# Optimization experiments

Hardware: AMD Instinct MI355X
Metric: run time of the kernel (lower is better)

## Reference

```python
import jax, jax.numpy as jnp
import numpy as np

SEG = 20  # patch size


def setup_inputs() -> dict:
    key = jax.random.key(0)
    k1, k2, k3, k4 = jax.random.split(key, 4)
    x = jax.random.uniform(k1, (2, 20, 1, 240, 240), dtype=jnp.float32)  # pixels in [0,1)
    emb_weight = jax.random.normal(k2, (256, 256), dtype=jnp.float32)
    pos_weight = jax.random.normal(k3, (144, 256), dtype=jnp.float32)
    temp_weight = jax.random.normal(k4, (20, 256), dtype=jnp.float32)
    return {"x": x, "emb_weight": emb_weight, "pos_weight": pos_weight, "temp_weight": temp_weight}


def reference(x, emb_weight, pos_weight, temp_weight):
    B, F, C, H, W = x.shape
    hp, wp = H // SEG, W // SEG  # 12, 12 -> 144 patches
    # segment_image: patches ordered row-major over (y, x), each patch flattened as [C, 20, 20]
    patches = x.reshape(B, F, C, hp, SEG, wp, SEG)
    patches = patches.transpose(0, 1, 3, 5, 2, 4, 6).reshape(B, F, hp * wp, C * SEG * SEG)
    idx = (patches * 255.0).astype(jnp.int32)          # truncation, matches .int()
    emb = emb_weight[idx].mean(axis=3)                 # [B, F, 144, 256] mean over pixels in patch
    emb = emb + pos_weight[None, None]                 # positional add
    cls = jnp.zeros((B, F, 1, emb.shape[-1]), emb.dtype)
    out = jnp.concatenate([cls, emb], axis=2)          # [B, F, 145, 256]
    out = out + temp_weight[:F][None, :, None, :]      # temporal add (incl. cls slot)
    return out
```

## Files before the change

kernel.cpp:

```cpp
#include <hip/hip_runtime.h>


#define F_   20
#define HW   240
#define SEG  20
#define PPB  8
#define BPF  18
#define NBLK (40 * BPF)

__device__ __forceinline__ float bf16_to_f32(ushort u) {
    union { uint i; float f; } c; c.i = ((uint)u) << 16; return c.f;
}
__device__ __forceinline__ ushort f32_to_bf16(float v) {
    union { float f; uint i; } c; c.f = v;
    uint u = c.i;
    u += 0x7FFFu + ((u >> 16) & 1u);
    return (ushort)(u >> 16);
}

template<bool BF16> __device__ __forceinline__ float load_in(const void* p, int i) {
    if constexpr (BF16) return bf16_to_f32(((const ushort*)p)[i]);
    else                return ((const float*)p)[i];
}
template<bool BF16> __device__ __forceinline__ void store_out(void* p, int i, float v) {
    if constexpr (BF16) ((ushort*)p)[i] = f32_to_bf16(v);
    else                ((float*)p)[i] = v;
}

__global__ void detect_dtype(const ushort* __restrict__ x, int* __restrict__ flag) {
    if (threadIdx.x == 0) {
        int bad = 0;
        for (int i = 0; i < 256; i += 2) bad += (int)(x[i] > 0x3F80u);
        *flag = (bad == 0) ? 1 : 0;
    }
}

template<bool BF16>
__device__ __forceinline__ void embed_body(
    const void* __restrict__ xg, const void* __restrict__ embg,
    const void* __restrict__ posg, const void* __restrict__ tempg,
    void* __restrict__ outg,
    uint (&cnt)[PPB][256], float (&cntf)[PPB][256])
{
    const int tid  = threadIdx.x;
    const int bf   = blockIdx.x / BPF;
    const int pblk = blockIdx.x % BPF;
    const int p0   = pblk * PPB;
    const int f    = bf % F_;

    #pragma unroll
    for (int i = 0; i < PPB; ++i) cnt[i][tid] = 0u;
    __syncthreads();

    const int xbase = bf * (HW * HW);
    for (int it = 0; it < 13; ++it) {
        int i = tid + it * 256;
        if (i < PPB * 400) {
            int p  = i / 400;
            int q  = i - p * 400;
            int gp = p0 + p;
            int pr = gp / 12, pc = gp - pr * 12;
            int qr = q / SEG, qc = q - qr * SEG;
            float xv = load_in<BF16>(xg, xbase + (pr * SEG + qr) * HW + pc * SEG + qc);
            int idx = (int)(xv * 255.0f);
            idx = idx < 0 ? 0 : (idx > 255 ? 255 : idx);
            atomicAdd(&cnt[p][idx], 1u);
        }
    }
    __syncthreads();

    #pragma unroll
    for (int i = 0; i < PPB; ++i) cntf[i][tid] = (float)cnt[i][tid];
    __syncthreads();

    float acc[PPB] = {};
    #pragma unroll 4
    for (int k = 0; k < 256; ++k) {
        float e = load_in<BF16>(embg, k * 256 + tid);
        #pragma unroll
        for (int m = 0; m < PPB; ++m) acc[m] += cntf[m][k] * e;
    }

    const int obase = bf * (145 * 256);
    const float tadd = load_in<BF16>(tempg, f * 256 + tid);
    if (pblk == 0)
        store_out<BF16>(outg, obase + tid, tadd);
    #pragma unroll
    for (int m = 0; m < PPB; ++m) {
        int gp = p0 + m;
        float val = acc[m] * (1.0f / 400.0f)
                  + load_in<BF16>(posg, gp * 256 + tid) + tadd;
        store_out<BF16>(outg, obase + (1 + gp) * 256 + tid, val);
    }
}

__global__ __launch_bounds__(256) void video_embed_kernel(
    const void* __restrict__ xg, const void* __restrict__ embg,
    const void* __restrict__ posg, const void* __restrict__ tempg,
    void* __restrict__ outg, const int* __restrict__ flag)
{
    __shared__ uint  cnt[PPB][256];
    __shared__ float cntf[PPB][256];
    const bool isbf = (flag == nullptr) ? true : (*flag != 0);
    if (isbf) embed_body<true >(xg, embg, posg, tempg, outg, cnt, cntf);
    else      embed_body<false>(xg, embg, posg, tempg, outg, cnt, cntf);
}

extern "C" void kernel_launch(void* const* d_in, const int* in_sizes, int n_in,
                              void* d_out, int out_size, void* d_ws, size_t ws_size,
                              hipStream_t stream) {
    int* flag = (ws_size >= sizeof(int)) ? (int*)d_ws : nullptr;
    if (flag)
        detect_dtype<<<dim3(1), dim3(64), 0, stream>>>((const ushort*)d_in[0], flag);
    video_embed_kernel<<<dim3(NBLK), dim3(256), 0, stream>>>(
        d_in[0], d_in[1], d_in[2], d_in[3], d_out, flag);
}
```

Measured before the change: 91.95 us.

## Process full patch-row strips per block with vectorized loads and register-tiled histogram GEMM

Each block now handles one full row of 12 patches (a contiguous 20x240 strip), so pixel loads are contiguous float4 reads and the histogram is accumulated directly as float atomics in LDS. The count-times-embedding product is register-tiled: each thread computes 4 output columns for 12 patches over a 64-wide k slice, and the four waves' partial sums are reduced through shared memory. The separate dtype-detection kernel launch is folded into the main kernel. In exchange, LDS use grows substantially (the per-wave partial buffer), which may reduce occupancy, and float atomics replace integer ones.

After: 91.75 us. Within noise of the previous version (-0.2%).

```diff
diff --git a/kernel.cpp b/kernel.cpp
--- a/kernel.cpp
+++ b/kernel.cpp
@@ -4,13 +4,17 @@
 #define F_   20
 #define HW   240
 #define SEG  20
-#define PPB  8
-#define BPF  18
+#define PPB  12
+#define BPF  12
 #define NBLK (40 * BPF)
+#define STRIP (HW * SEG)
 
-__device__ __forceinline__ float bf16_to_f32(ushort u) {
-    union { uint i; float f; } c; c.i = ((uint)u) << 16; return c.f;
+typedef __attribute__((ext_vector_type(4))) float float4_t;
+
+__device__ __forceinline__ float bits_f32(uint u) {
+    union { uint i; float f; } c; c.i = u; return c.f;
 }
+__device__ __forceinline__ float bf16_to_f32(ushort u) { return bits_f32(((uint)u) << 16); }
 __device__ __forceinline__ ushort f32_to_bf16(float v) {
     union { float f; uint i; } c; c.f = v;
     uint u = c.i;
@@ -18,100 +22,138 @@
     return (ushort)(u >> 16);
 }
 
-template<bool BF16> __device__ __forceinline__ float load_in(const void* p, int i) {
-    if constexpr (BF16) return bf16_to_f32(((const ushort*)p)[i]);
-    else                return ((const float*)p)[i];
+template<bool F32> __device__ __forceinline__ float4_t load4(const void* p, int i) {
+    if constexpr (F32) {
+        return *(const float4_t*)((const float*)p + i);
+    } else {
+        ushort4 u = *(const ushort4*)((const ushort*)p + i);
+        float4_t r;
+        r.x = bf16_to_f32(u.x); r.y = bf16_to_f32(u.y);
+        r.z = bf16_to_f32(u.z); r.w = bf16_to_f32(u.w);
+        return r;
+    }
 }
-template<bool BF16> __device__ __forceinline__ void store_out(void* p, int i, float v) {
-    if constexpr (BF16) ((ushort*)p)[i] = f32_to_bf16(v);
-    else                ((float*)p)[i] = v;
+template<bool F32> __device__ __forceinline__ float load1(const void* p, int i) {
+    if constexpr (F32) return ((const float*)p)[i];
+    else               return bf16_to_f32(((const ushort*)p)[i]);
+}
+template<bool F32> __device__ __forceinline__ void store1(void* p, int i, float v) {
+    if constexpr (F32) ((float*)p)[i] = v;
+    else               ((ushort*)p)[i] = f32_to_bf16(v);
 }
 
-__global__ void detect_dtype(const ushort* __restrict__ x, int* __restrict__ flag) {
-    if (threadIdx.x == 0) {
-        int bad = 0;
-        for (int i = 0; i < 256; i += 2) bad += (int)(x[i] > 0x3F80u);
-        *flag = (bad == 0) ? 1 : 0;
-    }
-}
-
-template<bool BF16>
+template<bool F32>
 __device__ __forceinline__ void embed_body(
     const void* __restrict__ xg, const void* __restrict__ embg,
     const void* __restrict__ posg, const void* __restrict__ tempg,
     void* __restrict__ outg,
-    uint (&cnt)[PPB][256], float (&cntf)[PPB][256])
+    float (&cntf)[PPB][256], float (&part)[PPB][4][256])
 {
     const int tid  = threadIdx.x;
+    const int lane = tid & 63;
+    const int wave = tid >> 6;
     const int bf   = blockIdx.x / BPF;
-    const int pblk = blockIdx.x % BPF;
-    const int p0   = pblk * PPB;
+    const int pr   = blockIdx.x % BPF;
+    const int p0   = pr * 12;
     const int f    = bf % F_;
 
-    #pragma unroll
-    for (int i = 0; i < PPB; ++i) cnt[i][tid] = 0u;
-    __syncthreads();
-
-    const int xbase = bf * (HW * HW);
-    for (int it = 0; it < 13; ++it) {
+    const int xbase = bf * (HW * HW) + pr * STRIP;
+    for (int it = 0; it < 5; ++it) {
         int i = tid + it * 256;
-        if (i < PPB * 400) {
-            int p  = i / 400;
-            int q  = i - p * 400;
-            int gp = p0 + p;
-            int pr = gp / 12, pc = gp - pr * 12;
-            int qr = q / SEG, qc = q - qr * SEG;
-            float xv = load_in<BF16>(xg, xbase + (pr * SEG + qr) * HW + pc * SEG + qc);
-            int idx = (int)(xv * 255.0f);
-            idx = idx < 0 ? 0 : (idx > 255 ? 255 : idx);
-            atomicAdd(&cnt[p][idx], 1u);
+        if (i < STRIP / 4) {
+            int elem = i * 4;
+            int col  = elem % HW;
+            int p    = col / SEG;
+            float4_t v = load4<F32>(xg, xbase + elem);
+            #pragma unroll
+            for (int j = 0; j < 4; ++j) {
+                int idx = (int)(v[j] * 255.0f);
+                idx = idx < 0 ? 0 : (idx > 255 ? 255 : idx);
+                atomicAdd(&cntf[p][idx], 1.0f);
+            }
         }
     }
     __syncthreads();
 
+    const int n0 = lane * 4;
+    const int kbase = wave * 64;
+    float acc[PPB][4];
     #pragma unroll
-    for (int i = 0; i < PPB; ++i) cntf[i][tid] = (float)cnt[i][tid];
+    for (int m = 0; m < PPB; ++m)
+        #pragma unroll
+        for (int c = 0; c < 4; ++c) acc[m][c] = 0.0f;
+
+    #pragma unroll 2
+    for (int kq = 0; kq < 16; ++kq) {
+        const int k = kbase + kq * 4;
+        float e[4][4];
+        #pragma unroll
+        for (int kk = 0; kk < 4; ++kk) {
+            if constexpr (F32) {
+                *(float4_t*)(&e[kk][0]) =
+                    *(const float4_t*)((const float*)embg + (k + kk) * 256 + n0);
+            } else {
+                uint2 u = *(const uint2*)((const ushort*)embg + (k + kk) * 256 + n0);
+                e[kk][0] = bits_f32(u.x << 16);
+                e[kk][1] = bits_f32(u.x & 0xFFFF0000u);
+                e[kk][2] = bits_f32(u.y << 16);
+                e[kk][3] = bits_f32(u.y & 0xFFFF0000u);
+            }
+        }
+        #pragma unroll
+        for (int m = 0; m < PPB; ++m) {
+            float4_t c4 = *(const float4_t*)(&cntf[m][k]);
+            #pragma unroll
+            for (int kk = 0; kk < 4; ++kk)
+                #pragma unroll
+                for (int c = 0; c < 4; ++c)
+                    acc[m][c] += c4[kk] * e[kk][c];
+        }
+    }
+
+    #pragma unroll
+    for (int m = 0; m < PPB; ++m)
+        *(float4_t*)(&part[m][wave][n0]) = *(float4_t*)(&acc[m][0]);
     __syncthreads();
 
-    float acc[PPB] = {};
-    #pragma unroll 4
-    for (int k = 0; k < 256; ++k) {
-        float e = load_in<BF16>(embg, k * 256 + tid);
-        #pragma unroll
-        for (int m = 0; m < PPB; ++m) acc[m] += cntf[m][k] * e;
-    }
-
     const int obase = bf * (145 * 256);
-    const float tadd = load_in<BF16>(tempg, f * 256 + tid);
-    if (pblk == 0)
-        store_out<BF16>(outg, obase + tid, tadd);
+    const float tadd = load1<F32>(tempg, f * 256 + tid);
+    if (pr == 0)
+        store1<F32>(outg, obase + tid, tadd);
     #pragma unroll
     for (int m = 0; m < PPB; ++m) {
+        float s = part[m][0][tid] + part[m][1][tid] + part[m][2][tid] + part[m][3][tid];
         int gp = p0 + m;
-        float val = acc[m] * (1.0f / 400.0f)
-                  + load_in<BF16>(posg, gp * 256 + tid) + tadd;
-        store_out<BF16>(outg, obase + (1 + gp) * 256 + tid, val);
+        float val = s * (1.0f / 400.0f) + load1<F32>(posg, gp * 256 + tid) + tadd;
+        store1<F32>(outg, obase + (1 + gp) * 256 + tid, val);
     }
 }
 
-__global__ __launch_bounds__(256) void video_embed_kernel(
+__global__ __launch_bounds__(256) void video_embed_v5_kernel(
     const void* __restrict__ xg, const void* __restrict__ embg,
     const void* __restrict__ posg, const void* __restrict__ tempg,
-    void* __restrict__ outg, const int* __restrict__ flag)
+    void* __restrict__ outg)
 {
-    __shared__ uint  cnt[PPB][256];
     __shared__ float cntf[PPB][256];
-    const bool isbf = (flag == nullptr) ? true : (*flag != 0);
-    if (isbf) embed_body<true >(xg, embg, posg, tempg, outg, cnt, cntf);
-    else      embed_body<false>(xg, embg, posg, tempg, outg, cnt, cntf);
+    __shared__ float part[PPB][4][256];
+    __shared__ int   isf32_s;
+
+    const int tid = threadIdx.x;
+    if (tid == 0) isf32_s = 0;
+    __syncthreads();
+
+    #pragma unroll
+    for (int i = 0; i < PPB; ++i) cntf[i][tid] = 0.0f;
+    if (tid < 128 && ((const ushort*)xg)[2 * tid] > 0x3F80u) isf32_s = 1;
+    __syncthreads();
+
+    if (isf32_s) embed_body<true >(xg, embg, posg, tempg, outg, cntf, part);
+    else         embed_body<false>(xg, embg, posg, tempg, outg, cntf, part);
 }
 
 extern "C" void kernel_launch(void* const* d_in, const int* in_sizes, int n_in,
                               void* d_out, int out_size, void* d_ws, size_t ws_size,
                               hipStream_t stream) {
-    int* flag = (ws_size >= sizeof(int)) ? (int*)d_ws : nullptr;
-    if (flag)
-        detect_dtype<<<dim3(1), dim3(64), 0, stream>>>((const ushort*)d_in[0], flag);
-    video_embed_kernel<<<dim3(NBLK), dim3(256), 0, stream>>>(
-        d_in[0], d_in[1], d_in[2], d_in[3], d_out, flag);
+    video_embed_v5_kernel<<<dim3(NBLK), dim3(256), 0, stream>>>(
+        d_in[0], d_in[1], d_in[2], d_in[3], d_out);
 }
```
